# Kernel optimization log

Measured on AMD Instinct MI355X. Metric: run time of the kernel, lower is better.

Reference implementation:

```python
import jax, jax.numpy as jnp
import numpy as np

B, D, K, E = 256, 256, 1024, 16  # batch, dim_codes, book_size, embedding_dim
DECAY = 0.999
GAIN = 1.0 - DECAY
EPS = 1e-6


def setup_inputs() -> dict:
    key = jax.random.key(0)
    k1, k2 = jax.random.split(key)
    return {
        "cw_q": jax.random.normal(k1, (B, D * E), dtype=jnp.float32),
        "codebook": jax.random.normal(k2, (D, K, E), dtype=jnp.float32),
        "ema_counts": jnp.ones((D, K), dtype=jnp.float32),
    }


def reference(cw_q, codebook, ema_counts):
    batch = cw_q.shape[0]
    x = cw_q.reshape(batch, D, E)  # [B, D, E]

    x2 = jnp.sum(x * x, axis=-1)                       # [B, D]
    c2 = jnp.sum(codebook * codebook, axis=-1)         # [D, K]
    xc = jnp.einsum('bde,dke->bdk', x, codebook)       # [B, D, K]
    dist = x2[:, :, None] + c2[None, :, :] - 2.0 * xc

    idx = jnp.argmin(dist, axis=-1)                    # [B, D] int32

    # gather nearest code vector per (batch, dim_code)
    cw_embed = codebook[jnp.arange(D)[None, :], idx]   # [B, D, E]
    cw_embed = cw_embed.reshape(batch, D * E)

    one_hot_idx = jax.nn.one_hot(idx, K, dtype=cw_q.dtype)  # [B, D, K]

    # EMA update (training path): scatter-sum of assigned vectors per code
    update = jnp.einsum('bdk,bde->dke', one_hot_idx, x)      # [D, K, E]
    new_codebook = codebook * DECAY + GAIN * update / (ema_counts[:, :, None] + EPS)
    new_ema_counts = DECAY * ema_counts + GAIN * jnp.sum(one_hot_idx, axis=0)

    return cw_embed, one_hot_idx, new_codebook, new_ema_counts
```

## Files before the change

### kernel.cpp

```cpp
#include <hip/hip_runtime.h>
#include <float.h>

#define BB 256
#define DD 256
#define KK 1024
#define EE 16
#define DECAY 0.999f
#define GAIN  0.001f
#define EPS   1e-6f

#define OH_OFF   ((size_t)BB * DD * EE)
#define CB_OFF   (OH_OFF + (size_t)BB * DD * KK)
#define EMA_OFF  (CB_OFF + (size_t)DD * KK * EE)

typedef float f32x4 __attribute__((ext_vector_type(4)));

__device__ __forceinline__ float dot16(const float4& a0, const float4& a1,
                                       const float4& a2, const float4& a3,
                                       const float4& b0, const float4& b1,
                                       const float4& b2, const float4& b3) {
  float s = a0.x * b0.x;
  s = fmaf(a0.y, b0.y, s); s = fmaf(a0.z, b0.z, s); s = fmaf(a0.w, b0.w, s);
  s = fmaf(a1.x, b1.x, s); s = fmaf(a1.y, b1.y, s); s = fmaf(a1.z, b1.z, s); s = fmaf(a1.w, b1.w, s);
  s = fmaf(a2.x, b2.x, s); s = fmaf(a2.y, b2.y, s); s = fmaf(a2.z, b2.z, s); s = fmaf(a2.w, b2.w, s);
  s = fmaf(a3.x, b3.x, s); s = fmaf(a3.y, b3.y, s); s = fmaf(a3.z, b3.z, s); s = fmaf(a3.w, b3.w, s);
  return s;
}

__device__ __forceinline__ unsigned long long packkey(float dist, int k) {
  unsigned u = __float_as_uint(dist);
  unsigned m = ((int)u < 0) ? 0xFFFFFFFFu : 0x80000000u;
  return ((unsigned long long)(u ^ m) << 32) | (unsigned long long)(unsigned)k;
}

__device__ __forceinline__ void ntst4(float4* p, float4 v) {
  f32x4 t = { v.x, v.y, v.z, v.w };
  __builtin_nontemporal_store(t, (f32x4*)p);
}

__global__ __launch_bounds__(1024) void vqvae_fused(
    const float* __restrict__ cw_q,
    const float* __restrict__ codebook,
    const float* __restrict__ ema,
    float* __restrict__ out)
{
  __shared__ float4 cb4s[KK * EE / 4];
  __shared__ float4 upd4s[KK * EE / 4];
  __shared__ float  c2s[KK];
  __shared__ float  esh[KK];
  __shared__ float  cnts[KK];
  __shared__ unsigned long long amin[BB];
  __shared__ int    ish[BB];

  const int t = threadIdx.x;
  const int d = blockIdx.x;
  const int w = t >> 6;
  const int l = t & 63;
  const float4 z4 = make_float4(0.f, 0.f, 0.f, 0.f);

  cnts[t] = 0.f;
  if (t < BB) amin[t] = ~0ULL;
  esh[t] = ema[(size_t)d * KK + t];
  #pragma unroll
  for (int i = 0; i < 4; ++i) upd4s[i * 1024 + t] = z4;

  const float4* src4 = (const float4*)codebook + (size_t)d * (KK * EE / 4);
  #pragma unroll
  for (int i = 0; i < 4; ++i) {
    int i4 = i * 1024 + t;
    float4 v = src4[i4];
    cb4s[i4] = v;
    float sq = v.x * v.x;
    sq = fmaf(v.y, v.y, sq);
    sq = fmaf(v.z, v.z, sq);
    sq = fmaf(v.w, v.w, sq);
    sq += __shfl_xor(sq, 1);
    sq += __shfl_xor(sq, 2);
    if ((t & 3) == 0) c2s[i4 >> 2] = sq;
  }

  float4 xv[4][4];
  float  x2[4];
  #pragma unroll
  for (int j = 0; j < 4; ++j) {
    const int b = l + 64 * j;
    const float4* xr = (const float4*)cw_q + (size_t)b * (DD * EE / 4) + d * 4;
    xv[j][0] = xr[0]; xv[j][1] = xr[1]; xv[j][2] = xr[2]; xv[j][3] = xr[3];
  }

  float* ohp = out + OH_OFF;
  float4* zb = (float4*)(ohp + (size_t)(w << 4) * (DD * KK) + (size_t)d * KK) + l;

  #pragma unroll
  for (int f = 0; f < 16; ++f)
    ntst4(&zb[(size_t)(f >> 2) * (DD * KK / 4) + (f & 3) * 64], z4);

  #pragma unroll
  for (int j = 0; j < 4; ++j)
    x2[j] = dot16(xv[j][0], xv[j][1], xv[j][2], xv[j][3],
                  xv[j][0], xv[j][1], xv[j][2], xv[j][3]);

  __syncthreads();

  float best[4] = {FLT_MAX, FLT_MAX, FLT_MAX, FLT_MAX};
  int   bi[4]   = {0, 0, 0, 0};
  const int kbase = w << 6;

  auto body = [&](int s) {
    const int k = kbase + s;
    const float4* p = cb4s + (k << 2);
    float4 c0 = p[0], c1 = p[1], c2v = p[2], c3 = p[3];
    const float c2k = c2s[k];
    #pragma unroll
    for (int j = 0; j < 4; ++j) {
      float dj = dot16(c0, c1, c2v, c3, xv[j][0], xv[j][1], xv[j][2], xv[j][3]);
      float dist = fmaf(-2.f, dj, x2[j] + c2k);
      if (dist < best[j]) { best[j] = dist; bi[j] = k; }
    }
  };

  #pragma unroll 1
  for (int s = 0; s < 48; ++s) {
    body(s);
    ntst4(&zb[(size_t)(4 + (s >> 2)) * (DD * KK / 4) + (s & 3) * 64], z4);
  }
  #pragma unroll 1
  for (int s = 48; s < 64; ++s) body(s);

  #pragma unroll
  for (int j = 0; j < 4; ++j)
    atomicMin(&amin[l + 64 * j], packkey(best[j], bi[j]));

  __syncthreads();

  const int e = t & 15;
  const int g = t >> 4;
  float xpre[4];
  #pragma unroll
  for (int i = 0; i < 4; ++i)
    xpre[i] = cw_q[(size_t)(g * 4 + i) * (DD * EE) + (size_t)d * EE + e];

  if (t < BB) {
    const int b = t;
    unsigned long long key = amin[b];
    const int bidx = (int)(unsigned)(key & 0xFFFFFFFFull);

    float4* ce = (float4*)out + (size_t)b * (DD * EE / 4) + d * 4;
    const float4* cwp = cb4s + (bidx << 2);
    ntst4(&ce[0], cwp[0]); ntst4(&ce[1], cwp[1]);
    ntst4(&ce[2], cwp[2]); ntst4(&ce[3], cwp[3]);

    __builtin_nontemporal_store(
        1.0f, &ohp[(size_t)b * (DD * KK) + (size_t)d * KK + bidx]);

    ish[b] = bidx;
    atomicAdd(&cnts[bidx], 1.0f);
  }
  __syncthreads();

  {
    float* upd = (float*)upd4s;
    #pragma unroll
    for (int i = 0; i < 4; ++i) {
      int k = ish[g * 4 + i];
      atomicAdd(&upd[k * EE + e], xpre[i]);
    }
    float* oe = out + EMA_OFF + (size_t)d * KK;
    __builtin_nontemporal_store(DECAY * esh[t] + GAIN * cnts[t], &oe[t]);
  }
  __syncthreads();

  {
    float4* ocb = (float4*)(out + CB_OFF) + (size_t)d * (KK * EE / 4);
    #pragma unroll
    for (int i = 0; i < 4; ++i) {
      int i4 = i * 1024 + t;
      int k  = i4 >> 2;
      float4 c = cb4s[i4];
      float4 u = upd4s[i4];
      float inv = GAIN / (esh[k] + EPS);
      float4 r;
      r.x = DECAY * c.x + u.x * inv;
      r.y = DECAY * c.y + u.y * inv;
      r.z = DECAY * c.z + u.z * inv;
      r.w = DECAY * c.w + u.w * inv;
      ntst4(&ocb[i4], r);
    }
  }
}

extern "C" void kernel_launch(void* const* d_in, const int* in_sizes, int n_in,
                              void* d_out, int out_size, void* d_ws, size_t ws_size,
                              hipStream_t stream) {
  const float* cw_q     = (const float*)d_in[0];
  const float* codebook = (const float*)d_in[1];
  const float* ema      = (const float*)d_in[2];
  float* out = (float*)d_out;
  (void)in_sizes; (void)n_in; (void)out_size; (void)d_ws; (void)ws_size;

  vqvae_fused<<<dim3(DD), dim3(1024), 0, stream>>>(cw_q, codebook, ema, out);
}
```

Measured before the change: 318.1 us.

## Split one-hot fill into a separate row-contiguous kernel using stashed indices

The main kernel no longer zero-fills the 256 MB one-hot tensor with strided per-d writes. It stores each argmin index in the first slots of the corresponding one-hot row. A second kernel, one block per batch row, reads those indices into shared memory and writes each contiguous row of one-hot values in one pass. This makes the dominant output write fully sequential, but it adds a kernel launch and a dependency on the stashed indices being read before they are overwritten. The argmin loop is also simplified into a single loop with unroll 2.

```diff
diff --git a/kernel.cpp b/kernel.cpp
--- a/kernel.cpp
+++ b/kernel.cpp
@@ -38,7 +38,7 @@
   __builtin_nontemporal_store(t, (f32x4*)p);
 }
 
-__global__ __launch_bounds__(1024) void vqvae_fused(
+__global__ __launch_bounds__(1024) void vqvae_main(
     const float* __restrict__ cw_q,
     const float* __restrict__ codebook,
     const float* __restrict__ ema,
@@ -87,14 +87,6 @@
     const float4* xr = (const float4*)cw_q + (size_t)b * (DD * EE / 4) + d * 4;
     xv[j][0] = xr[0]; xv[j][1] = xr[1]; xv[j][2] = xr[2]; xv[j][3] = xr[3];
   }
-
-  float* ohp = out + OH_OFF;
-  float4* zb = (float4*)(ohp + (size_t)(w << 4) * (DD * KK) + (size_t)d * KK) + l;
-
-  #pragma unroll
-  for (int f = 0; f < 16; ++f)
-    ntst4(&zb[(size_t)(f >> 2) * (DD * KK / 4) + (f & 3) * 64], z4);
-
   #pragma unroll
   for (int j = 0; j < 4; ++j)
     x2[j] = dot16(xv[j][0], xv[j][1], xv[j][2], xv[j][3],
@@ -106,7 +98,8 @@
   int   bi[4]   = {0, 0, 0, 0};
   const int kbase = w << 6;
 
-  auto body = [&](int s) {
+  #pragma unroll 2
+  for (int s = 0; s < 64; ++s) {
     const int k = kbase + s;
     const float4* p = cb4s + (k << 2);
     float4 c0 = p[0], c1 = p[1], c2v = p[2], c3 = p[3];
@@ -117,16 +110,7 @@
       float dist = fmaf(-2.f, dj, x2[j] + c2k);
       if (dist < best[j]) { best[j] = dist; bi[j] = k; }
     }
-  };
-
-  #pragma unroll 1
-  for (int s = 0; s < 48; ++s) {
-    body(s);
-    ntst4(&zb[(size_t)(4 + (s >> 2)) * (DD * KK / 4) + (s & 3) * 64], z4);
-  }
-  #pragma unroll 1
-  for (int s = 48; s < 64; ++s) body(s);
-
+  }
   #pragma unroll
   for (int j = 0; j < 4; ++j)
     atomicMin(&amin[l + 64 * j], packkey(best[j], bi[j]));
@@ -150,8 +134,7 @@
     ntst4(&ce[0], cwp[0]); ntst4(&ce[1], cwp[1]);
     ntst4(&ce[2], cwp[2]); ntst4(&ce[3], cwp[3]);
 
-    __builtin_nontemporal_store(
-        1.0f, &ohp[(size_t)b * (DD * KK) + (size_t)d * KK + bidx]);
+    ((int*)(out + OH_OFF))[(size_t)b * (DD * KK) + d] = bidx;
 
     ish[b] = bidx;
     atomicAdd(&cnts[bidx], 1.0f);
@@ -189,6 +172,32 @@
   }
 }
 
+__global__ __launch_bounds__(1024) void vqvae_onehot(float* __restrict__ out)
+{
+  __shared__ int ksh[DD];
+  const int b = blockIdx.x;
+  const int t = threadIdx.x;
+  float* row = out + OH_OFF + (size_t)b * (DD * KK);
+
+  if (t < DD) ksh[t] = ((const int*)row)[t];
+  __syncthreads();
+
+  float4* row4 = (float4*)row;
+  const int rel = (t & 255) << 2;
+  const int tq  = t >> 8;
+
+  #pragma unroll 4
+  for (int i = 0; i < 64; ++i) {
+    const int hot = ksh[i * 4 + tq];
+    float4 v;
+    v.x = (rel     == hot) ? 1.0f : 0.0f;
+    v.y = (rel + 1 == hot) ? 1.0f : 0.0f;
+    v.z = (rel + 2 == hot) ? 1.0f : 0.0f;
+    v.w = (rel + 3 == hot) ? 1.0f : 0.0f;
+    ntst4(&row4[i * 1024 + t], v);
+  }
+}
+
 extern "C" void kernel_launch(void* const* d_in, const int* in_sizes, int n_in,
                               void* d_out, int out_size, void* d_ws, size_t ws_size,
                               hipStream_t stream) {
@@ -198,5 +207,6 @@
   float* out = (float*)d_out;
   (void)in_sizes; (void)n_in; (void)out_size; (void)d_ws; (void)ws_size;
 
-  vqvae_fused<<<dim3(DD), dim3(1024), 0, stream>>>(cw_q, codebook, ema, out);
-}
+  vqvae_main<<<dim3(DD), dim3(1024), 0, stream>>>(cw_q, codebook, ema, out);
+  vqvae_onehot<<<dim3(BB), dim3(1024), 0, stream>>>(out);
+}
```

Result: slower. 341.2 us (+7.3%).
